# Optimization experiments

Measured on AMD Instinct MI355X. Metric: run time of the kernel, lower is better.

The kernel has to match this reference:

```python
import jax, jax.numpy as jnp
import numpy as np

H = 8          # num_heads
DIM = 1024     # embed dim
DH = DIM // H // 2   # per-branch head dim = 64
B, N = 2, 2048
LAMBDA_INIT = 0.5
COS_MIN, COS_MAX = 0.0, 15.0
ALPHA = 0.5            # cos_head_residual_alpha
COS_EPS = 1e-6
RMS_EPS = 1e-5
# raw init so that sigmoid(raw) = (cos_scale_init - min)/(max - min) = 1/15
RAW_INIT = float(np.log((1.0/15.0) / (1.0 - 1.0/15.0)))


def setup_inputs() -> dict:
    key = jax.random.key(0)
    ks = jax.random.split(key, 10)
    s = 1.0 / np.sqrt(DIM)
    return {
        "x": jax.random.normal(ks[0], (B, N, DIM), jnp.float32),
        "Wq": jax.random.normal(ks[1], (DIM, DIM), jnp.float32) * s,
        "Wk": jax.random.normal(ks[2], (DIM, DIM), jnp.float32) * s,
        "Wv": jax.random.normal(ks[3], (DIM, DIM), jnp.float32) * s,
        "Wo": jax.random.normal(ks[4], (DIM, DIM), jnp.float32) * s,
        "bo": jnp.zeros((DIM,), jnp.float32),
        "lambda_q1": jax.random.normal(ks[5], (DH,), jnp.float32) * 0.1,
        "lambda_k1": jax.random.normal(ks[6], (DH,), jnp.float32) * 0.1,
        "lambda_q2": jax.random.normal(ks[7], (DH,), jnp.float32) * 0.1,
        "lambda_k2": jax.random.normal(ks[8], (DH,), jnp.float32) * 0.1,
        "delta_gain": jax.random.normal(ks[9], (H,), jnp.float32) * 0.1,
        "cos_head_delta": jnp.zeros((H,), jnp.float32),
        "cos_logit_scale_raw": jnp.float32(RAW_INIT),
        "subln_weight": jnp.ones((2 * DH,), jnp.float32),
    }


def _l2norm(t):
    # F.normalize: x / max(||x||_2, eps)
    return t / jnp.maximum(jnp.linalg.norm(t, axis=-1, keepdims=True), COS_EPS)


def reference(x, Wq, Wk, Wv, Wo, bo,
              lambda_q1, lambda_k1, lambda_q2, lambda_k2,
              delta_gain, cos_head_delta, cos_logit_scale_raw, subln_weight):
    b, n, c = x.shape
    # projections (torch Linear: x @ W.T)
    q = (x @ Wq.T).reshape(b, n, H, 2, DH).transpose(0, 2, 3, 1, 4)  # (B,H,2,N,Dh)
    k = (x @ Wk.T).reshape(b, n, H, 2, DH).transpose(0, 2, 3, 1, 4)
    v = (x @ Wv.T).reshape(b, n, H, 2 * DH).transpose(0, 2, 1, 3)    # (B,H,N,2Dh)
    q1, q2 = q[:, :, 0], q[:, :, 1]
    k1, k2 = k[:, :, 0], k[:, :, 1]

    # smooth-bounded cosine logit scale with per-head residual
    gscale = COS_MIN + (COS_MAX - COS_MIN) * jax.nn.sigmoid(cos_logit_scale_raw)
    head_delta = cos_head_delta - cos_head_delta.mean()
    cos_scale = (gscale * (1.0 + ALPHA * jnp.tanh(head_delta))).reshape(1, H, 1, 1)

    L1 = jnp.einsum('bhnd,bhmd->bhnm', _l2norm(q1), _l2norm(k1)) * cos_scale
    L2 = jnp.einsum('bhnd,bhmd->bhnm', _l2norm(q2), _l2norm(k2)) * cos_scale
    L1 = jnp.nan_to_num(L1)
    L2 = jnp.nan_to_num(L2)

    # tanh-gated interaction between branches
    G = jnp.tanh(delta_gain.reshape(1, H, 1, 1) * (L1 - L2))
    A1 = jax.nn.softmax((L1 + G).astype(jnp.float32), axis=-1).astype(x.dtype)
    A2 = jax.nn.softmax((L2 - G).astype(jnp.float32), axis=-1).astype(x.dtype)

    lambda_1 = jnp.exp(jnp.sum(lambda_q1 * lambda_k1))
    lambda_2 = jnp.exp(jnp.sum(lambda_q2 * lambda_k2))
    lambda_full = (lambda_1 - lambda_2 + LAMBDA_INIT).astype(x.dtype)

    attn = A1 - lambda_full * A2
    y = jnp.einsum('bhnm,bhmd->bhnd', attn, v)  # (B,H,N,2Dh)

    # sub-layer RMSNorm over last dim (2*Dh) with affine weight
    y = y * jax.lax.rsqrt(jnp.mean(y * y, axis=-1, keepdims=True) + RMS_EPS) * subln_weight
    y = y * (1.0 - LAMBDA_INIT)

    y = y.transpose(0, 2, 1, 3).reshape(b, n, c)
    return y @ Wo.T + bo
```

## Files before the change

### kernel.cpp

```cpp
#include <hip/hip_runtime.h>
#include <hip/hip_bf16.h>
#include <cstdint>

typedef __attribute__((ext_vector_type(8))) short short8_t;
typedef __attribute__((ext_vector_type(4))) float f32x4;
typedef __attribute__((ext_vector_type(16))) float f32x16;

#define LOG2E 1.4426950408889634f

__device__ __forceinline__ ushort f2bf(float f){
  union { float f; uint32_t i; } x; x.f = f;
  uint32_t r = x.i + 0x7FFFu + ((x.i >> 16) & 1u);
  return (ushort)(r >> 16);
}
__device__ __forceinline__ float fexp2(float x){
  float r; asm("v_exp_f32 %0, %1" : "=v"(r) : "v"(x)); return r;
}
__device__ __forceinline__ uint32_t cvtpk_bf16(float lo, float hi){
  uint32_t r;
  asm("v_cvt_pk_bf16_f32 %0, %1, %2" : "=v"(r) : "v"(lo), "v"(hi));
  return r;
}
__device__ __forceinline__ void pl32swap(uint32_t &a, uint32_t &b){
  asm volatile("v_permlane32_swap_b32 %0, %1" : "+v"(a), "+v"(b));
}
union PF { uint32_t u[4]; short8_t v; };

__global__ __launch_bounds__(256) void cvt_all_kernel(const float* __restrict__ x,
                                                      const float* __restrict__ Wq,
                                                      const float* __restrict__ Wk,
                                                      const float* __restrict__ Wv,
                                                      const float* __restrict__ Wo,
                                                      ushort* __restrict__ xb,
                                                      ushort* __restrict__ wqb,
                                                      ushort* __restrict__ wkb,
                                                      ushort* __restrict__ wvb,
                                                      ushort* __restrict__ wob){
  int bid = blockIdx.x;
  const float* s; ushort* d; int i;
  if (bid < 4096){ s = x; d = xb; i = bid * 256 + threadIdx.x; }
  else {
    int sel = (bid - 4096) >> 10;
    s = sel == 0 ? Wq : sel == 1 ? Wk : sel == 2 ? Wv : Wo;
    d = sel == 0 ? wqb : sel == 1 ? wkb : sel == 2 ? wvb : wob;
    i = ((bid - 4096) & 1023) * 256 + threadIdx.x;
  }
  float4 v = ((const float4*)s)[i];
  ushort4 o;
  o.x = f2bf(v.x); o.y = f2bf(v.y); o.z = f2bf(v.z); o.w = f2bf(v.w);
  ((ushort4*)d)[i] = o;
}

__global__ void prep_kernel(const float* __restrict__ lq1, const float* __restrict__ lk1,
                            const float* __restrict__ lq2, const float* __restrict__ lk2,
                            const float* __restrict__ dgain, const float* __restrict__ chd,
                            const float* __restrict__ rawp, float* __restrict__ sc){
  int lane = threadIdx.x;
  float p1 = lq1[lane] * lk1[lane];
  float p2 = lq2[lane] * lk2[lane];
  #pragma unroll
  for (int o = 1; o < 64; o <<= 1){
    p1 += __shfl_xor(p1, o, 64);
    p2 += __shfl_xor(p2, o, 64);
  }
  if (lane == 0) sc[24] = expf(p1) - expf(p2) + 0.5f;
  if (lane < 8){
    float m = 0.f;
    for (int i = 0; i < 8; i++) m += chd[i];
    m *= 0.125f;
    float gs = 15.f / (1.f + expf(-rawp[0]));
    float cs = gs * (1.f + 0.5f * tanhf(chd[lane] - m));
    sc[lane]      = LOG2E * cs;
    sc[8 + lane]  = LOG2E * (cs + 1.f);
    sc[16 + lane] = 2.f * dgain[lane];
  }
}

__global__ __launch_bounds__(256) void gemm_qkv(const ushort* __restrict__ A,
                                                const ushort* __restrict__ wqb,
                                                const ushort* __restrict__ wkb,
                                                const ushort* __restrict__ wvb,
                                                ushort* __restrict__ Qs,
                                                ushort* __restrict__ Kn,
                                                ushort* __restrict__ Vt,
                                                const float* __restrict__ sc){
  constexpr int N = 1024, K = 1024;
  __shared__ ushort As[128*32];
  __shared__ ushort Bs[128*32];
  const int z = blockIdx.z;
  const ushort* Bm = z == 0 ? wqb : (z == 1 ? wkb : wvb);
  const int t = threadIdx.x;
  const int lane = t & 63;
  const int w = t >> 6;
  const int wr = w >> 1, wc = w & 1;
  const long Ar0 = (long)blockIdx.x * 128;
  const long Br0 = (long)blockIdx.y * 128;
  const int r15 = lane & 15;
  const int kb = (lane >> 4) * 8;

  f32x4 acc[4][4];
  #pragma unroll
  for (int m = 0; m < 4; m++)
    #pragma unroll
    for (int n = 0; n < 4; n++) acc[m][n] = (f32x4){0.f, 0.f, 0.f, 0.f};

  for (int k0 = 0; k0 < K; k0 += 32){
    __syncthreads();
    #pragma unroll
    for (int r = 0; r < 2; r++){
      int li = r * 256 + t;
      int row = li >> 2;
      int col = (li & 3) * 8;
      __builtin_amdgcn_global_load_lds(
        (const __attribute__((address_space(1))) uint32_t*)(A + (Ar0 + row) * K + k0 + col),
        (__attribute__((address_space(3))) uint32_t*)(As + li * 8), 16, 0, 0);
      __builtin_amdgcn_global_load_lds(
        (const __attribute__((address_space(1))) uint32_t*)(Bm + (Br0 + row) * K + k0 + col),
        (__attribute__((address_space(3))) uint32_t*)(Bs + li * 8), 16, 0, 0);
    }
    __syncthreads();
    short8_t af[4], bfv[4];
    #pragma unroll
    for (int m = 0; m < 4; m++) af[m]  = *(const short8_t*)(As + (wr*64 + m*16 + r15)*32 + kb);
    #pragma unroll
    for (int n = 0; n < 4; n++) bfv[n] = *(const short8_t*)(Bs + (wc*64 + n*16 + r15)*32 + kb);
    #pragma unroll
    for (int m = 0; m < 4; m++)
      #pragma unroll
      for (int n = 0; n < 4; n++)
        acc[m][n] = __builtin_amdgcn_mfma_f32_16x16x32_bf16(af[m], bfv[n], acc[m][n], 0, 0, 0);
  }

  const int fr = (lane >> 4) * 4;
  if (z == 2){
    #pragma unroll
    for (int m = 0; m < 4; m++){
      #pragma unroll
      for (int n = 0; n < 4; n++){
        long row0 = Ar0 + wr*64 + m*16 + fr;
        long col  = Br0 + wc*64 + n*16 + r15;
        int bidx = (int)(row0 >> 11);
        int tok  = (int)(row0 & 2047);
        int hh   = (int)(col >> 7);
        int dd   = (int)(col & 127);
        ushort4 pk;
        pk.x = f2bf(acc[m][n][0]); pk.y = f2bf(acc[m][n][1]);
        pk.z = f2bf(acc[m][n][2]); pk.w = f2bf(acc[m][n][3]);
        *(ushort4*)(Vt + ((long)((bidx*8 + hh)*128 + dd))*2048 + tok) = pk;
      }
    }
  } else {
    ushort* dst = (z == 0) ? Qs : Kn;
    const float qsc = (z == 0) ? sc[Br0 >> 7] : 1.f;
    #pragma unroll
    for (int m = 0; m < 4; m++){
      float ss[4] = {0.f, 0.f, 0.f, 0.f};
      #pragma unroll
      for (int n = 0; n < 4; n++)
        #pragma unroll
        for (int r = 0; r < 4; r++) ss[r] = fmaf(acc[m][n][r], acc[m][n][r], ss[r]);
      #pragma unroll
      for (int r = 0; r < 4; r++){
        ss[r] += __shfl_xor(ss[r], 1, 16);
        ss[r] += __shfl_xor(ss[r], 2, 16);
        ss[r] += __shfl_xor(ss[r], 4, 16);
        ss[r] += __shfl_xor(ss[r], 8, 16);
        ss[r] = qsc / fmaxf(sqrtf(ss[r]), 1e-6f);
      }
      long row0 = Ar0 + wr*64 + m*16 + fr;
      #pragma unroll
      for (int n = 0; n < 4; n++){
        long col = Br0 + wc*64 + n*16 + r15;
        #pragma unroll
        for (int r = 0; r < 4; r++)
          dst[(row0 + r) * N + col] = f2bf(acc[m][n][r] * ss[r]);
      }
    }
  }
}

__global__ __launch_bounds__(256) void gemm_o(const ushort* __restrict__ A,
                                              const ushort* __restrict__ Bm,
                                              float* __restrict__ Cout,
                                              const float* __restrict__ bias){
  constexpr int N = 1024, K = 1024;
  __shared__ ushort As[128*32];
  __shared__ ushort Bs[128*32];
  const int t = threadIdx.x;
  const int lane = t & 63;
  const int w = t >> 6;
  const int wr = w >> 1, wc = w & 1;
  const long Ar0 = (long)blockIdx.x * 128;
  const long Br0 = (long)blockIdx.y * 128;
  const int r15 = lane & 15;
  const int kb = (lane >> 4) * 8;

  f32x4 acc[4][4];
  #pragma unroll
  for (int m = 0; m < 4; m++)
    #pragma unroll
    for (int n = 0; n < 4; n++) acc[m][n] = (f32x4){0.f, 0.f, 0.f, 0.f};

  for (int k0 = 0; k0 < K; k0 += 32){
    __syncthreads();
    #pragma unroll
    for (int r = 0; r < 2; r++){
      int li = r * 256 + t;
      int row = li >> 2;
      int col = (li & 3) * 8;
      __builtin_amdgcn_global_load_lds(
        (const __attribute__((address_space(1))) uint32_t*)(A + (Ar0 + row) * K + k0 + col),
        (__attribute__((address_space(3))) uint32_t*)(As + li * 8), 16, 0, 0);
      __builtin_amdgcn_global_load_lds(
        (const __attribute__((address_space(1))) uint32_t*)(Bm + (Br0 + row) * K + k0 + col),
        (__attribute__((address_space(3))) uint32_t*)(Bs + li * 8), 16, 0, 0);
    }
    __syncthreads();
    short8_t af[4], bfv[4];
    #pragma unroll
    for (int m = 0; m < 4; m++) af[m]  = *(const short8_t*)(As + (wr*64 + m*16 + r15)*32 + kb);
    #pragma unroll
    for (int n = 0; n < 4; n++) bfv[n] = *(const short8_t*)(Bs + (wc*64 + n*16 + r15)*32 + kb);
    #pragma unroll
    for (int m = 0; m < 4; m++)
      #pragma unroll
      for (int n = 0; n < 4; n++)
        acc[m][n] = __builtin_amdgcn_mfma_f32_16x16x32_bf16(af[m], bfv[n], acc[m][n], 0, 0, 0);
  }

  const int fr = (lane >> 4) * 4;
  #pragma unroll
  for (int m = 0; m < 4; m++){
    #pragma unroll
    for (int n = 0; n < 4; n++){
      long row0 = Ar0 + wr*64 + m*16 + fr;
      long col  = Br0 + wc*64 + n*16 + r15;
      float bsv = bias[col];
      #pragma unroll
      for (int r = 0; r < 4; r++)
        Cout[(row0 + r) * N + col] = acc[m][n][r] + bsv;
    }
  }
}

__device__ __forceinline__ void stage_tile(const ushort* __restrict__ Kn,
                                           const ushort* __restrict__ Vt,
                                           long kslice, long vslice, int kt,
                                           ushort* buf, int t){
  #pragma unroll
  for (int r = 0; r < 8; r++){
    int s = r * 128 + t;
    int key = s >> 4, ci = s & 15;
    const ushort* srcK = Kn + kslice + (long)(kt + key) * 1024 + ((ci ^ (key & 15)) * 8);
    __builtin_amdgcn_global_load_lds(
      (const __attribute__((address_space(1))) uint32_t*)srcK,
      (__attribute__((address_space(3))) uint32_t*)(buf + s * 8), 16, 0, 0);
    int dim = s >> 3, ci2 = s & 7;
    const ushort* srcV = Vt + vslice + (long)dim * 2048 + kt + ((ci2 ^ (dim & 7)) * 8);
    __builtin_amdgcn_global_load_lds(
      (const __attribute__((address_space(1))) uint32_t*)srcV,
      (__attribute__((address_space(3))) uint32_t*)(buf + 64*128 + s * 8), 16, 0, 0);
  }
}

__global__ __launch_bounds__(128, 1) void attn4_kernel(
    const ushort* __restrict__ Qs, const ushort* __restrict__ Kn,
    const ushort* __restrict__ Vt, ushort* __restrict__ Yb,
    const float* __restrict__ sc, const float* __restrict__ subw){
  __shared__ ushort KV2[2][64*128 + 128*64];
  const int t = threadIdx.x;
  const int w = t >> 6;
  const int l = t & 63;
  const int lo5 = l & 31;
  const int hi = l >> 5;
  const int bh = blockIdx.y;
  const int b = bh >> 3, h = bh & 7;
  const int q0 = blockIdx.x * 64 + w * 32;
  const float dgh2 = sc[16 + h];
  const float shl  = sc[8 + h];
  const float lam  = sc[24];

  short8_t qf[8];
  {
    const ushort* qp = Qs + (long)(b*2048 + q0 + lo5) * 1024 + h*128 + hi*8;
    #pragma unroll
    for (int c = 0; c < 2; c++)
      #pragma unroll
      for (int kc = 0; kc < 4; kc++)
        qf[c*4 + kc] = *(const short8_t*)(qp + c*64 + kc*16);
  }

  f32x16 y1a[4], y2a[4];
  #pragma unroll
  for (int nt = 0; nt < 4; nt++)
    #pragma unroll
    for (int i = 0; i < 16; i++){ y1a[nt][i] = 0.f; y2a[nt][i] = 0.f; }
  float Z1 = 0.f, Z2 = 0.f;

  const long kslice = (long)b * 2048 * 1024 + h * 128;
  const long vslice = (long)(b*8 + h) * 128 * 2048;

  stage_tile(Kn, Vt, kslice, vslice, 0, KV2[0], t);
  int ib = 0;
  for (int kt = 0; kt < 2048; kt += 64, ib ^= 1){
    __syncthreads();
    if (kt + 64 < 2048) stage_tile(Kn, Vt, kslice, vslice, kt + 64, KV2[ib ^ 1], t);
    const ushort* Ks = KV2[ib];
    const ushort* Vs = KV2[ib] + 64*128;

    #pragma unroll
    for (int step = 0; step < 2; step++){
      const int key = step*32 + lo5;
      const int krow = key * 128;
      const int ksw = key & 15;
      f32x16 s1, s2;
      #pragma unroll
      for (int i = 0; i < 16; i++){ s1[i] = 0.f; s2[i] = 0.f; }
      #pragma unroll
      for (int kc = 0; kc < 4; kc++){
        short8_t kf = *(const short8_t*)(Ks + krow + (((kc*2 + hi) ^ ksw) * 8));
        s1 = __builtin_amdgcn_mfma_f32_32x32x16_bf16(kf, qf[kc], s1, 0, 0, 0);
      }
      #pragma unroll
      for (int kc = 0; kc < 4; kc++){
        short8_t kf = *(const short8_t*)(Ks + krow + (((8 + kc*2 + hi) ^ ksw) * 8));
        s2 = __builtin_amdgcn_mfma_f32_32x32x16_bf16(kf, qf[4 + kc], s2, 0, 0, 0);
      }

      uint32_t pa1[8], pa2[8];
      #pragma unroll
      for (int ks = 0; ks < 2; ks++){
        #pragma unroll
        for (int u = 0; u < 2; u++){
          const int rr = 8*ks + 2*u;
          float e1[4], e2[4];
          #pragma unroll
          for (int g4 = 0; g4 < 4; g4++){
            const int r = rr + (g4 >> 1)*4 + (g4 & 1);
            float a = s1[r], c = s2[r];
            float e  = fexp2(dgh2 * (a - c));
            float rc = __builtin_amdgcn_rcpf(e + 1.f);
            float gl = fmaf(-2.f * LOG2E, rc, LOG2E);
            float p1 = fexp2(a + gl - shl);
            float p2 = fexp2(c - gl - shl);
            Z1 += p1; Z2 += p2;
            e1[g4] = p1; e2[g4] = p2;
          }
          uint32_t a1 = cvtpk_bf16(e1[0], e1[1]), b1 = cvtpk_bf16(e1[2], e1[3]);
          uint32_t a2 = cvtpk_bf16(e2[0], e2[1]), b2 = cvtpk_bf16(e2[2], e2[3]);
          pl32swap(a1, b1);
          pl32swap(a2, b2);
          pa1[ks*4 + u] = a1; pa1[ks*4 + 2 + u] = b1;
          pa2[ks*4 + u] = a2; pa2[ks*4 + 2 + u] = b2;
        }
      }

      #pragma unroll
      for (int ks = 0; ks < 2; ks++){
        PF f1, f2;
        #pragma unroll
        for (int i = 0; i < 4; i++){ f1.u[i] = pa1[ks*4 + i]; f2.u[i] = pa2[ks*4 + i]; }
        const int ck = step*4 + ks*2 + hi;
        #pragma unroll
        for (int nt = 0; nt < 4; nt++){
          const int dim = nt*32 + lo5;
          short8_t vf = *(const short8_t*)(Vs + dim*64 + ((ck ^ (dim & 7)) * 8));
          y1a[nt] = __builtin_amdgcn_mfma_f32_32x32x16_bf16(f1.v, vf, y1a[nt], 0, 0, 0);
          y2a[nt] = __builtin_amdgcn_mfma_f32_32x32x16_bf16(f2.v, vf, y2a[nt], 0, 0, 0);
        }
      }
    }
  }

  Z1 += __shfl_xor(Z1, 32, 64);
  Z2 += __shfl_xor(Z2, 32, 64);
  #pragma unroll
  for (int r = 0; r < 16; r++){
    const int qr = (r & 3) + 8*(r >> 2) + 4*hi;
    float z1r = __shfl(Z1, (l & 32) | qr, 64);
    float z2r = __shfl(Z2, (l & 32) | qr, 64);
    float inv1 = 1.f / z1r;
    float inv2 = lam / z2r;
    float yv[4]; float ssq = 0.f;
    #pragma unroll
    for (int nt = 0; nt < 4; nt++){
      yv[nt] = y1a[nt][r]*inv1 - y2a[nt][r]*inv2;
      ssq = fmaf(yv[nt], yv[nt], ssq);
    }
    ssq += __shfl_xor(ssq, 1, 64);
    ssq += __shfl_xor(ssq, 2, 64);
    ssq += __shfl_xor(ssq, 4, 64);
    ssq += __shfl_xor(ssq, 8, 64);
    ssq += __shfl_xor(ssq, 16, 64);
    float rms = rsqrtf(ssq * (1.f / 128.f) + 1e-5f);
    const long tok = (long)b*2048 + q0 + qr;
    ushort* op = Yb + tok*1024 + h*128;
    #pragma unroll
    for (int nt = 0; nt < 4; nt++){
      const int dim = nt*32 + lo5;
      op[dim] = f2bf(yv[nt] * rms * subw[dim] * 0.5f);
    }
  }
}

extern "C" void kernel_launch(void* const* d_in, const int* in_sizes, int n_in,
                              void* d_out, int out_size, void* d_ws, size_t ws_size,
                              hipStream_t stream) {
  const float* x   = (const float*)d_in[0];
  const float* Wq  = (const float*)d_in[1];
  const float* Wk  = (const float*)d_in[2];
  const float* Wv  = (const float*)d_in[3];
  const float* Wo  = (const float*)d_in[4];
  const float* bo  = (const float*)d_in[5];
  const float* lq1 = (const float*)d_in[6];
  const float* lk1 = (const float*)d_in[7];
  const float* lq2 = (const float*)d_in[8];
  const float* lk2 = (const float*)d_in[9];
  const float* dg  = (const float*)d_in[10];
  const float* chd = (const float*)d_in[11];
  const float* raw = (const float*)d_in[12];
  const float* subw= (const float*)d_in[13];
  float* out = (float*)d_out;

  char* ws = (char*)d_ws;
  const size_t MB = 1024 * 1024;
  ushort* xb  = (ushort*)(ws);
  ushort* wqb = (ushort*)(ws + 8 * MB);
  ushort* wkb = wqb + 1024 * 1024;
  ushort* wvb = wkb + 1024 * 1024;
  ushort* wob = wvb + 1024 * 1024;
  ushort* Qs  = (ushort*)(ws + 16 * MB);
  ushort* Kn  = Qs + 4 * 1024 * 1024;
  ushort* Vt  = Kn + 4 * 1024 * 1024;
  ushort* Yb  = Vt + 4 * 1024 * 1024;
  float*  sc  = (float*)(Yb + 4 * 1024 * 1024);

  cvt_all_kernel<<<8192, 256, 0, stream>>>(x, Wq, Wk, Wv, Wo, xb, wqb, wkb, wvb, wob);
  prep_kernel<<<1, 64, 0, stream>>>(lq1, lk1, lq2, lk2, dg, chd, raw, sc);

  gemm_qkv<<<dim3(32, 8, 3), 256, 0, stream>>>(xb, wqb, wkb, wvb, Qs, Kn, Vt, sc);

  attn4_kernel<<<dim3(32, 16), 128, 0, stream>>>(Qs, Kn, Vt, Yb, sc, subw);

  gemm_o<<<dim3(32, 8), 256, 0, stream>>>(Yb, wob, out, bo);
}
```

Baseline: 183.3 us.

## Split attention key range across two wave pairs with LDS reduction

The attention kernel goes from 128 to 256 threads. Each pair of waves now handles half of the key sequence for the same 32 query rows, and the partial outputs and normalisers are merged through shared memory at the end. The aim is to double the waves per block so latency is hidden better, given only 512 blocks on the device. In exchange, the double-buffered prefetch pipeline is dropped: each iteration loads both halves and then synchronises before computing, so load latency is no longer overlapped. The LDS reduction of the accumulators also adds a cost at the end.

```diff
diff --git a/kernel.cpp b/kernel.cpp
--- a/kernel.cpp
+++ b/kernel.cpp
@@ -243,39 +243,42 @@
   }
 }
 
-__device__ __forceinline__ void stage_tile(const ushort* __restrict__ Kn,
-                                           const ushort* __restrict__ Vt,
-                                           long kslice, long vslice, int kt,
-                                           ushort* buf, int t){
-  #pragma unroll
-  for (int r = 0; r < 8; r++){
-    int s = r * 128 + t;
+__device__ __forceinline__ void stage256(const ushort* __restrict__ Kn,
+                                         const ushort* __restrict__ Vt,
+                                         long kslice, long vslice, int ktAbs,
+                                         ushort* buf, int t){
+  #pragma unroll
+  for (int r = 0; r < 4; r++){
+    int s = r * 256 + t;
     int key = s >> 4, ci = s & 15;
-    const ushort* srcK = Kn + kslice + (long)(kt + key) * 1024 + ((ci ^ (key & 15)) * 8);
+    const ushort* srcK = Kn + kslice + (long)(ktAbs + key) * 1024 + ((ci ^ (key & 15)) * 8);
     __builtin_amdgcn_global_load_lds(
       (const __attribute__((address_space(1))) uint32_t*)srcK,
       (__attribute__((address_space(3))) uint32_t*)(buf + s * 8), 16, 0, 0);
     int dim = s >> 3, ci2 = s & 7;
-    const ushort* srcV = Vt + vslice + (long)dim * 2048 + kt + ((ci2 ^ (dim & 7)) * 8);
+    const ushort* srcV = Vt + vslice + (long)dim * 2048 + ktAbs + ((ci2 ^ (dim & 7)) * 8);
     __builtin_amdgcn_global_load_lds(
       (const __attribute__((address_space(1))) uint32_t*)srcV,
       (__attribute__((address_space(3))) uint32_t*)(buf + 64*128 + s * 8), 16, 0, 0);
   }
 }
 
-__global__ __launch_bounds__(128, 1) void attn4_kernel(
+__global__ __launch_bounds__(256, 2) void attn5_kernel(
     const ushort* __restrict__ Qs, const ushort* __restrict__ Kn,
     const ushort* __restrict__ Vt, ushort* __restrict__ Yb,
     const float* __restrict__ sc, const float* __restrict__ subw){
-  __shared__ ushort KV2[2][64*128 + 128*64];
+  __shared__ ushort KV[2][64*128 + 128*64];
+  __shared__ float Zb[2][2][64];
   const int t = threadIdx.x;
   const int w = t >> 6;
   const int l = t & 63;
   const int lo5 = l & 31;
   const int hi = l >> 5;
+  const int qt = w >> 1;
+  const int kp = w & 1;
   const int bh = blockIdx.y;
   const int b = bh >> 3, h = bh & 7;
-  const int q0 = blockIdx.x * 64 + w * 32;
+  const int q0 = blockIdx.x * 64 + qt * 32;
   const float dgh2 = sc[16 + h];
   const float shl  = sc[8 + h];
   const float lam  = sc[24];
@@ -300,13 +303,13 @@
   const long kslice = (long)b * 2048 * 1024 + h * 128;
   const long vslice = (long)(b*8 + h) * 128 * 2048;
 
-  stage_tile(Kn, Vt, kslice, vslice, 0, KV2[0], t);
-  int ib = 0;
-  for (int kt = 0; kt < 2048; kt += 64, ib ^= 1){
-    __syncthreads();
-    if (kt + 64 < 2048) stage_tile(Kn, Vt, kslice, vslice, kt + 64, KV2[ib ^ 1], t);
-    const ushort* Ks = KV2[ib];
-    const ushort* Vs = KV2[ib] + 64*128;
+  for (int kt0 = 0; kt0 < 1024; kt0 += 64){
+    __syncthreads();
+    stage256(Kn, Vt, kslice, vslice, kt0,        KV[0], t);
+    stage256(Kn, Vt, kslice, vslice, 1024 + kt0, KV[1], t);
+    __syncthreads();
+    const ushort* Ks = KV[kp];
+    const ushort* Vs = KV[kp] + 64*128;
 
     #pragma unroll
     for (int step = 0; step < 2; step++){
@@ -374,6 +377,32 @@
 
   Z1 += __shfl_xor(Z1, 32, 64);
   Z2 += __shfl_xor(Z2, 32, 64);
+
+  __syncthreads();
+  float* Mb = (float*)(&KV[0][0]);
+  if (kp == 1){
+    #pragma unroll
+    for (int nt = 0; nt < 4; nt++)
+      #pragma unroll
+      for (int i = 0; i < 16; i++){
+        Mb[(((qt*2 + 0)*4 + nt)*16 + i)*64 + l] = y1a[nt][i];
+        Mb[(((qt*2 + 1)*4 + nt)*16 + i)*64 + l] = y2a[nt][i];
+      }
+    Zb[qt][0][l] = Z1; Zb[qt][1][l] = Z2;
+  }
+  __syncthreads();
+  if (kp == 1) return;
+
+  #pragma unroll
+  for (int nt = 0; nt < 4; nt++)
+    #pragma unroll
+    for (int i = 0; i < 16; i++){
+      y1a[nt][i] += Mb[(((qt*2 + 0)*4 + nt)*16 + i)*64 + l];
+      y2a[nt][i] += Mb[(((qt*2 + 1)*4 + nt)*16 + i)*64 + l];
+    }
+  Z1 += Zb[qt][0][l];
+  Z2 += Zb[qt][1][l];
+
   #pragma unroll
   for (int r = 0; r < 16; r++){
     const int qr = (r & 3) + 8*(r >> 2) + 4*hi;
@@ -440,7 +469,7 @@
 
   gemm_qkv<<<dim3(32, 8, 3), 256, 0, stream>>>(xb, wqb, wkb, wvb, Qs, Kn, Vt, sc);
 
-  attn4_kernel<<<dim3(32, 16), 128, 0, stream>>>(Qs, Kn, Vt, Yb, sc, subw);
+  attn5_kernel<<<dim3(32, 16), 256, 0, stream>>>(Qs, Kn, Vt, Yb, sc, subw);
 
   gemm_o<<<dim3(32, 8), 256, 0, stream>>>(Yb, wob, out, bo);
 }
```

New measurement: 164.1 us. 1.12x faster.
